# Kernel optimization log

Measured on AMD Instinct MI355X. Metric: run time of the kernel, lower is better.

Reference implementation:

```python
import jax, jax.numpy as jnp
import numpy as np

IN_F = 4096
OUT_F = 11008
N_CLUSTERS = 16
TOPK = int(IN_F * 0.25)  # 1024


def setup_inputs() -> dict:
    key = jax.random.key(0)
    k1, k2, k3, k4 = jax.random.split(key, 4)
    x = jax.random.normal(k1, (1, 1, IN_F), jnp.float32)
    weight_full = jax.random.normal(k2, (OUT_F, IN_F), jnp.float32) * 0.02
    bias_full = jax.random.normal(k3, (OUT_F,), jnp.float32) * 0.02
    # cluster centers live in softmax-activation space (compared via cdist to a softmax)
    cluster_centers = jax.nn.softmax(
        jax.random.normal(k4, (N_CLUSTERS, IN_F), jnp.float32), axis=-1)
    return {"x": x, "weight_full": weight_full, "bias_full": bias_full,
            "cluster_centers": cluster_centers}


def reference(x, weight_full, bias_full, cluster_centers):
    # hot path: bsz * seq == 1
    x_flat = x.reshape(-1, x.shape[-1])                 # [1, in]
    x_avg = jnp.abs(jnp.mean(x_flat, axis=0))           # [in]
    activation = jax.nn.softmax(x_avg, axis=0)          # [in]
    # nearest cluster center (squared L2 has same argmin as L2)
    d2 = jnp.sum((cluster_centers - activation[None, :]) ** 2, axis=-1)  # [n_clusters]
    ci = jnp.argmin(d2)
    center = cluster_centers[ci]                        # [in]
    # per-cluster precomputed top-k column indices: argsort(center, descending)[:topk]
    _, topk_idx = jax.lax.top_k(center, TOPK)           # [topk]
    x_sel = jnp.take(x_flat, topk_idx, axis=1)          # [1, topk]
    w_sel = jnp.take(weight_full, topk_idx, axis=1)     # [out, topk]
    out = x_sel @ w_sel.T + bias_full                   # [1, out]
    return out.reshape(1, 1, -1)
```

## Files before the change

### kernel.cpp

```cpp
#include <hip/hip_runtime.h>

#define IN_F 4096
#define OUT_F 11008
#define NCLUST 16
#define TOPK 1024
#define NT 1024
#define NW 16

__global__ __launch_bounds__(NT) void select_mask_kernel(
    const float* __restrict__ x,
    const float* __restrict__ centers,
    float* __restrict__ xm)
{
    const int tid  = threadIdx.x;
    const int lane = tid & 63;
    const int wid  = tid >> 6;

    __shared__ __align__(16) float sx[IN_F];
    __shared__ __align__(16) float sact[IN_F];
    __shared__ unsigned int hist[NW * 256];
    __shared__ float swred[NW];
    __shared__ float sd2[NCLUST];
    __shared__ unsigned int wtot4[4];
    __shared__ unsigned int weq[NW];
    __shared__ float smax, ssum;
    __shared__ unsigned int sprefix, sKrem, sG;
    __shared__ int sci;

    if (tid == 0) { sprefix = 0u; sKrem = TOPK; sG = 0u; }

    float4 xv = reinterpret_cast<const float4*>(x)[tid];
    reinterpret_cast<float4*>(sx)[tid] = xv;
    {
        float m = fmaxf(fmaxf(fabsf(xv.x), fabsf(xv.y)),
                        fmaxf(fabsf(xv.z), fabsf(xv.w)));
        for (int off = 32; off > 0; off >>= 1) m = fmaxf(m, __shfl_down(m, off, 64));
        if (lane == 0) swred[wid] = m;
    }
    __syncthreads();
    if (wid == 0) {
        float m = (lane < NW) ? swred[lane] : -3.0e38f;
        for (int off = 8; off > 0; off >>= 1) m = fmaxf(m, __shfl_down(m, off, 64));
        if (lane == 0) smax = m;
    }
    __syncthreads();
    const float mx = smax;

    float e0 = expf(fabsf(xv.x) - mx);
    float e1 = expf(fabsf(xv.y) - mx);
    float e2 = expf(fabsf(xv.z) - mx);
    float e3 = expf(fabsf(xv.w) - mx);
    {
        float s = e0 + e1 + e2 + e3;
        for (int off = 32; off > 0; off >>= 1) s += __shfl_down(s, off, 64);
        if (lane == 0) swred[wid] = s;
    }
    __syncthreads();
    if (wid == 0) {
        float s = (lane < NW) ? swred[lane] : 0.0f;
        for (int off = 8; off > 0; off >>= 1) s += __shfl_down(s, off, 64);
        if (lane == 0) ssum = s;
    }
    __syncthreads();
    {
        const float inv = 1.0f / ssum;
        float4 a;
        a.x = e0 * inv; a.y = e1 * inv; a.z = e2 * inv; a.w = e3 * inv;
        reinterpret_cast<float4*>(sact)[tid] = a;
    }
    __syncthreads();

    {
        const float4* c4 = reinterpret_cast<const float4*>(centers + (size_t)wid * IN_F);
        const float4* a4 = reinterpret_cast<const float4*>(sact);
        float d = 0.0f;
        #pragma unroll
        for (int it = 0; it < IN_F / 4 / 64; ++it) {
            float4 c = c4[it * 64 + lane];
            float4 a = a4[it * 64 + lane];
            float t0 = c.x - a.x, t1 = c.y - a.y, t2 = c.z - a.z, t3 = c.w - a.w;
            d += t0 * t0 + t1 * t1 + t2 * t2 + t3 * t3;
        }
        for (int off = 32; off > 0; off >>= 1) d += __shfl_down(d, off, 64);
        if (lane == 0) sd2[wid] = d;
    }
    __syncthreads();

    if (wid == 0) {
        float v = (lane < NCLUST) ? sd2[lane] : 3.0e38f;
        int   bi = lane;
        for (int off = 8; off > 0; off >>= 1) {
            float ov = __shfl_down(v, off, 64);
            int   oi = __shfl_down(bi, off, 64);
            if (ov < v) { v = ov; bi = oi; }
        }
        if (lane == 0) sci = bi;
    }
    __syncthreads();

    unsigned int cv[4];
    {
        float4 c = reinterpret_cast<const float4*>(centers + (size_t)sci * IN_F)[tid];
        cv[0] = __float_as_uint(c.x);
        cv[1] = __float_as_uint(c.y);
        cv[2] = __float_as_uint(c.z);
        cv[3] = __float_as_uint(c.w);
    }

    for (int pass = 0; pass < 4; ++pass) {
        const int shift = 24 - 8 * pass;
        for (int k = tid; k < NW * 256; k += NT) hist[k] = 0u;
        __syncthreads();
        const unsigned int pfx  = sprefix;
        const unsigned int krem = sKrem;
        unsigned int* hp = &hist[wid * 256];
        #pragma unroll
        for (int j = 0; j < 4; ++j) {
            unsigned int u = cv[j];
            bool cand = (pass == 0) || ((u >> (shift + 8)) == pfx);
            if (cand) atomicAdd(&hp[(u >> shift) & 255u], 1u);
        }
        __syncthreads();
        unsigned int h = 0, s = 0;
        if (tid < 256) {
            #pragma unroll
            for (int w = 0; w < NW; ++w) h += hist[w * 256 + tid];
            s = h;
            for (int off = 1; off < 64; off <<= 1) {
                unsigned int v2 = __shfl_down(s, off, 64);
                if (lane + off < 64) s += v2;
            }
            if (lane == 0) wtot4[wid] = s;
        }
        __syncthreads();
        if (tid < 256) {
            unsigned int add = 0;
            #pragma unroll
            for (int w = 0; w < 4; ++w) if (w > wid) add += wtot4[w];
            unsigned int incl = s + add;
            unsigned int excl = incl - h;
            if (excl < krem && krem <= incl) {
                sprefix = (pfx << 8) | (unsigned int)tid;
                sKrem   = krem - excl;
            }
        }
        __syncthreads();
    }
    const unsigned int T = sprefix;

    unsigned int gt = 0, eq = 0;
    #pragma unroll
    for (int j = 0; j < 4; ++j) {
        gt += (cv[j] > T) ? 1u : 0u;
        eq += (cv[j] == T) ? 1u : 0u;
    }
    {
        unsigned int g = gt;
        for (int off = 32; off > 0; off >>= 1) g += __shfl_down(g, off, 64);
        if (lane == 0) atomicAdd(&sG, g);
    }
    unsigned int p = eq;
    for (int off = 1; off < 64; off <<= 1) {
        unsigned int v2 = __shfl_up(p, off, 64);
        if (lane >= off) p += v2;
    }
    if (lane == 63) weq[wid] = p;
    __syncthreads();
    unsigned int base = p - eq;
    #pragma unroll
    for (int w = 0; w < NW; ++w) if (w < wid) base += weq[w];
    const unsigned int needEq = TOPK - sG;

    {
        unsigned int r = 0;
        float4 o;
        o.x = ((cv[0] > T) || ((cv[0] == T) && (base + r < needEq))) ? xv.x : 0.0f; r += (cv[0] == T);
        o.y = ((cv[1] > T) || ((cv[1] == T) && (base + r < needEq))) ? xv.y : 0.0f; r += (cv[1] == T);
        o.z = ((cv[2] > T) || ((cv[2] == T) && (base + r < needEq))) ? xv.z : 0.0f; r += (cv[2] == T);
        o.w = ((cv[3] > T) || ((cv[3] == T) && (base + r < needEq))) ? xv.w : 0.0f;
        reinterpret_cast<float4*>(xm)[tid] = o;
    }
}

__global__ __launch_bounds__(256) void matvec_kernel(
    const float* __restrict__ W,
    const float* __restrict__ xm,
    const float* __restrict__ bias,
    float* __restrict__ out)
{
    __shared__ __align__(16) float sxm[IN_F];
    const int tid = threadIdx.x;
    for (int i = tid * 4; i < IN_F; i += 256 * 4) {
        *reinterpret_cast<float4*>(&sxm[i]) =
            *reinterpret_cast<const float4*>(&xm[i]);
    }
    __syncthreads();

    const int lane = tid & 63;
    const int wid  = tid >> 6;
    const int nwaves = gridDim.x * 4;

    for (int row = blockIdx.x * 4 + wid; row < OUT_F; row += nwaves) {
        const float4* wr = reinterpret_cast<const float4*>(W + (size_t)row * IN_F);
        float acc = 0.0f;
        #pragma unroll
        for (int j = 0; j < IN_F / 4 / 64; ++j) {
            float4 w4 = wr[j * 64 + lane];
            float4 x4 = *reinterpret_cast<const float4*>(&sxm[(j * 64 + lane) * 4]);
            acc += w4.x * x4.x + w4.y * x4.y + w4.z * x4.z + w4.w * x4.w;
        }
        for (int off = 32; off > 0; off >>= 1) acc += __shfl_down(acc, off, 64);
        if (lane == 0) out[row] = acc + bias[row];
    }
}

extern "C" void kernel_launch(void* const* d_in, const int* in_sizes, int n_in,
                              void* d_out, int out_size, void* d_ws, size_t ws_size,
                              hipStream_t stream) {
    const float* x       = (const float*)d_in[0];
    const float* weight  = (const float*)d_in[1];
    const float* bias    = (const float*)d_in[2];
    const float* centers = (const float*)d_in[3];
    float* out = (float*)d_out;
    float* xm  = (float*)d_ws;

    select_mask_kernel<<<1, NT, 0, stream>>>(x, centers, xm);
    matvec_kernel<<<1376, 256, 0, stream>>>(weight, xm, bias, out);
}
```

Before: 45.65 us.

## Prefetch centers, expand cluster distance algebraically, process two rows per wave

The selection kernel now loads each wave's cluster center into registers at the start. It computes the nearest cluster as ||c||^2 - (2/sum)·c·e, using the unnormalised exponentials, which removes the softmax normalisation pass and several barriers. The chosen center is then reused from registers through shared memory instead of being re-read from global memory, and histogram clearing is moved to cut barriers. The matvec kernel has each wave compute two rows at once with independent loads, which raises memory-level parallelism in place of the strided row loop. The new launch bound with 64 float4 registers per thread risks register spills in the selection kernel, and the algebraic expansion can change rounding near ties.

```diff
diff --git a/kernel.cpp b/kernel.cpp
--- a/kernel.cpp
+++ b/kernel.cpp
@@ -7,7 +7,7 @@
 #define NT 1024
 #define NW 16
 
-__global__ __launch_bounds__(NT) void select_mask_kernel(
+__global__ __launch_bounds__(NT, 4) void select_mask_kernel(
     const float* __restrict__ x,
     const float* __restrict__ centers,
     float* __restrict__ xm)
@@ -16,21 +16,27 @@
     const int lane = tid & 63;
     const int wid  = tid >> 6;
 
-    __shared__ __align__(16) float sx[IN_F];
     __shared__ __align__(16) float sact[IN_F];
     __shared__ unsigned int hist[NW * 256];
     __shared__ float swred[NW];
-    __shared__ float sd2[NCLUST];
+    __shared__ float sdot[NCLUST];
+    __shared__ float scsq[NCLUST];
     __shared__ unsigned int wtot4[4];
     __shared__ unsigned int weq[NW];
-    __shared__ float smax, ssum;
+    __shared__ float smax;
     __shared__ unsigned int sprefix, sKrem, sG;
     __shared__ int sci;
 
     if (tid == 0) { sprefix = 0u; sKrem = TOPK; sG = 0u; }
 
     float4 xv = reinterpret_cast<const float4*>(x)[tid];
-    reinterpret_cast<float4*>(sx)[tid] = xv;
+    float4 cpre[16];
+    {
+        const float4* c4 = reinterpret_cast<const float4*>(centers + (size_t)wid * IN_F);
+        #pragma unroll
+        for (int it = 0; it < 16; ++it) cpre[it] = c4[it * 64 + lane];
+    }
+
     {
         float m = fmaxf(fmaxf(fabsf(xv.x), fabsf(xv.y)),
                         fmaxf(fabsf(xv.z), fabsf(xv.w)));
@@ -51,44 +57,38 @@
     float e2 = expf(fabsf(xv.z) - mx);
     float e3 = expf(fabsf(xv.w) - mx);
     {
+        float4 ev; ev.x = e0; ev.y = e1; ev.z = e2; ev.w = e3;
+        reinterpret_cast<float4*>(sact)[tid] = ev;
         float s = e0 + e1 + e2 + e3;
         for (int off = 32; off > 0; off >>= 1) s += __shfl_down(s, off, 64);
         if (lane == 0) swred[wid] = s;
     }
     __syncthreads();
+
+    {
+        const float4* a4 = reinterpret_cast<const float4*>(sact);
+        float dt = 0.0f, cq = 0.0f;
+        #pragma unroll
+        for (int it = 0; it < 16; ++it) {
+            float4 c = cpre[it];
+            float4 a = a4[it * 64 + lane];
+            dt += c.x * a.x + c.y * a.y + c.z * a.z + c.w * a.w;
+            cq += c.x * c.x + c.y * c.y + c.z * c.z + c.w * c.w;
+        }
+        for (int off = 32; off > 0; off >>= 1) {
+            dt += __shfl_down(dt, off, 64);
+            cq += __shfl_down(cq, off, 64);
+        }
+        if (lane == 0) { sdot[wid] = dt; scsq[wid] = cq; }
+    }
+    __syncthreads();
+
     if (wid == 0) {
         float s = (lane < NW) ? swred[lane] : 0.0f;
         for (int off = 8; off > 0; off >>= 1) s += __shfl_down(s, off, 64);
-        if (lane == 0) ssum = s;
-    }
-    __syncthreads();
-    {
-        const float inv = 1.0f / ssum;
-        float4 a;
-        a.x = e0 * inv; a.y = e1 * inv; a.z = e2 * inv; a.w = e3 * inv;
-        reinterpret_cast<float4*>(sact)[tid] = a;
-    }
-    __syncthreads();
-
-    {
-        const float4* c4 = reinterpret_cast<const float4*>(centers + (size_t)wid * IN_F);
-        const float4* a4 = reinterpret_cast<const float4*>(sact);
-        float d = 0.0f;
-        #pragma unroll
-        for (int it = 0; it < IN_F / 4 / 64; ++it) {
-            float4 c = c4[it * 64 + lane];
-            float4 a = a4[it * 64 + lane];
-            float t0 = c.x - a.x, t1 = c.y - a.y, t2 = c.z - a.z, t3 = c.w - a.w;
-            d += t0 * t0 + t1 * t1 + t2 * t2 + t3 * t3;
-        }
-        for (int off = 32; off > 0; off >>= 1) d += __shfl_down(d, off, 64);
-        if (lane == 0) sd2[wid] = d;
-    }
-    __syncthreads();
-
-    if (wid == 0) {
-        float v = (lane < NCLUST) ? sd2[lane] : 3.0e38f;
-        int   bi = lane;
+        s = __shfl(s, 0, 64);
+        float v = (lane < NCLUST) ? (scsq[lane] - (2.0f / s) * sdot[lane]) : 3.0e38f;
+        int bi = lane;
         for (int off = 8; off > 0; off >>= 1) {
             float ov = __shfl_down(v, off, 64);
             int   oi = __shfl_down(bi, off, 64);
@@ -98,9 +98,17 @@
     }
     __syncthreads();
 
+    if (wid == sci) {
+        float4* a4 = reinterpret_cast<float4*>(sact);
+        #pragma unroll
+        for (int it = 0; it < 16; ++it) a4[it * 64 + lane] = cpre[it];
+    }
+    for (int k = tid; k < NW * 256; k += NT) hist[k] = 0u;
+    __syncthreads();
+
     unsigned int cv[4];
     {
-        float4 c = reinterpret_cast<const float4*>(centers + (size_t)sci * IN_F)[tid];
+        float4 c = reinterpret_cast<const float4*>(sact)[tid];
         cv[0] = __float_as_uint(c.x);
         cv[1] = __float_as_uint(c.y);
         cv[2] = __float_as_uint(c.z);
@@ -109,8 +117,6 @@
 
     for (int pass = 0; pass < 4; ++pass) {
         const int shift = 24 - 8 * pass;
-        for (int k = tid; k < NW * 256; k += NT) hist[k] = 0u;
-        __syncthreads();
         const unsigned int pfx  = sprefix;
         const unsigned int krem = sKrem;
         unsigned int* hp = &hist[wid * 256];
@@ -145,6 +151,10 @@
             }
         }
         __syncthreads();
+        if (pass < 3) {
+            for (int k = tid; k < NW * 256; k += NT) hist[k] = 0u;
+            __syncthreads();
+        }
     }
     const unsigned int T = sprefix;
 
@@ -190,27 +200,39 @@
 {
     __shared__ __align__(16) float sxm[IN_F];
     const int tid = threadIdx.x;
-    for (int i = tid * 4; i < IN_F; i += 256 * 4) {
-        *reinterpret_cast<float4*>(&sxm[i]) =
-            *reinterpret_cast<const float4*>(&xm[i]);
+    {
+        const float4* src = reinterpret_cast<const float4*>(xm);
+        float4* dst = reinterpret_cast<float4*>(sxm);
+        #pragma unroll
+        for (int i = 0; i < IN_F / 4 / 256; ++i)
+            dst[i * 256 + tid] = src[i * 256 + tid];
     }
     __syncthreads();
 
     const int lane = tid & 63;
     const int wid  = tid >> 6;
-    const int nwaves = gridDim.x * 4;
-
-    for (int row = blockIdx.x * 4 + wid; row < OUT_F; row += nwaves) {
-        const float4* wr = reinterpret_cast<const float4*>(W + (size_t)row * IN_F);
-        float acc = 0.0f;
-        #pragma unroll
-        for (int j = 0; j < IN_F / 4 / 64; ++j) {
-            float4 w4 = wr[j * 64 + lane];
-            float4 x4 = *reinterpret_cast<const float4*>(&sxm[(j * 64 + lane) * 4]);
-            acc += w4.x * x4.x + w4.y * x4.y + w4.z * x4.z + w4.w * x4.w;
-        }
-        for (int off = 32; off > 0; off >>= 1) acc += __shfl_down(acc, off, 64);
-        if (lane == 0) out[row] = acc + bias[row];
+    const int r0 = blockIdx.x * 8 + wid * 2;
+
+    const float4* w0 = reinterpret_cast<const float4*>(W + (size_t)r0 * IN_F);
+    const float4* w1 = reinterpret_cast<const float4*>(W + (size_t)(r0 + 1) * IN_F);
+    const float4* x4 = reinterpret_cast<const float4*>(sxm);
+
+    float acc0 = 0.0f, acc1 = 0.0f;
+    #pragma unroll
+    for (int j = 0; j < IN_F / 4 / 64; ++j) {
+        float4 a = w0[j * 64 + lane];
+        float4 b = w1[j * 64 + lane];
+        float4 v = x4[j * 64 + lane];
+        acc0 += a.x * v.x + a.y * v.y + a.z * v.z + a.w * v.w;
+        acc1 += b.x * v.x + b.y * v.y + b.z * v.z + b.w * v.w;
+    }
+    for (int off = 32; off > 0; off >>= 1) {
+        acc0 += __shfl_down(acc0, off, 64);
+        acc1 += __shfl_down(acc1, off, 64);
+    }
+    if (lane == 0) {
+        out[r0]     = acc0 + bias[r0];
+        out[r0 + 1] = acc1 + bias[r0 + 1];
     }
 }
 
```

Measured after the change: 45.40 us. Within noise of the previous version (-0.5%).

## Fuse mask selection into matvec with redundant per-block selection and LDS-staged weight prefetch

Applied to the files above, without the earlier changes.

Merges the single-block selection kernel and the matvec into one 256-block kernel. Every block recomputes the softmax, nearest-center search and radix top-k itself. The cluster distance is rewritten as ||c||^2 - 2/S·(c·e), which skips the normalisation pass. Weight rows are streamed into LDS with global_load_lds double buffering and manual vmcnt waits, and the first granules are issued before the selection work so the loads overlap it. This removes a kernel launch and the serial single-block stage, at the cost of redundant selection work in every block and fragile hand-written waitcnt pipelining.

```diff
diff --git a/kernel.cpp b/kernel.cpp
--- a/kernel.cpp
+++ b/kernel.cpp
@@ -4,91 +4,134 @@
 #define OUT_F 11008
 #define NCLUST 16
 #define TOPK 1024
-#define NT 1024
-#define NW 16
-
-__global__ __launch_bounds__(NT) void select_mask_kernel(
+#define NBLK 256
+#define ROWS_PB 43
+#define GRAN_F 1024
+
+__device__ __forceinline__ float dot4(float4 a, float4 b) {
+    return a.x * b.x + a.y * b.y + a.z * b.z + a.w * b.w;
+}
+__device__ __forceinline__ float wredsum(float v) {
+    for (int o = 32; o > 0; o >>= 1) v += __shfl_down(v, o, 64);
+    return v;
+}
+__device__ __forceinline__ float wredmax(float v) {
+    for (int o = 32; o > 0; o >>= 1) v = fmaxf(v, __shfl_down(v, o, 64));
+    return v;
+}
+__device__ __forceinline__ void barrier_lds() {
+    asm volatile("s_waitcnt lgkmcnt(0)" ::: "memory");
+    __builtin_amdgcn_s_barrier();
+}
+__device__ __forceinline__ void stage_granule(const float* __restrict__ W,
+                                              int row, int q, float* lbuf,
+                                              int lane) {
+    const float* src = W + (size_t)row * IN_F + q * GRAN_F + lane * 4;
+    #pragma unroll
+    for (int j = 0; j < 4; ++j) {
+        __builtin_amdgcn_global_load_lds(
+            (const __attribute__((address_space(1))) void*)(src + j * 256),
+            (__attribute__((address_space(3))) void*)(lbuf + j * 256),
+            16, 0, 0);
+    }
+}
+
+__global__ __launch_bounds__(256, 1) void fused_kernel(
     const float* __restrict__ x,
+    const float* __restrict__ W,
+    const float* __restrict__ bias,
     const float* __restrict__ centers,
-    float* __restrict__ xm)
+    float* __restrict__ out)
 {
     const int tid  = threadIdx.x;
     const int lane = tid & 63;
     const int wid  = tid >> 6;
-
-    __shared__ __align__(16) float sx[IN_F];
-    __shared__ __align__(16) float sact[IN_F];
-    __shared__ unsigned int hist[NW * 256];
-    __shared__ float swred[NW];
-    __shared__ float sd2[NCLUST];
-    __shared__ unsigned int wtot4[4];
-    __shared__ unsigned int weq[NW];
-    __shared__ float smax, ssum;
+    const int bid  = blockIdx.x;
+
+    __shared__ __align__(16) float sxm[IN_F];
+    __shared__ __align__(16) float wstage[8][GRAN_F];
+    __shared__ unsigned int hist[4][256];
+    __shared__ float sredA[4], sredB[4];
+    __shared__ float sdot[NCLUST], scsq[NCLUST];
+    __shared__ unsigned int wtot4[4], weq[4];
     __shared__ unsigned int sprefix, sKrem, sG;
     __shared__ int sci;
 
-    if (tid == 0) { sprefix = 0u; sKrem = TOPK; sG = 0u; }
-
-    float4 xv = reinterpret_cast<const float4*>(x)[tid];
-    reinterpret_cast<float4*>(sx)[tid] = xv;
-    {
-        float m = fmaxf(fmaxf(fabsf(xv.x), fabsf(xv.y)),
-                        fmaxf(fabsf(xv.z), fabsf(xv.w)));
-        for (int off = 32; off > 0; off >>= 1) m = fmaxf(m, __shfl_down(m, off, 64));
-        if (lane == 0) swred[wid] = m;
-    }
-    __syncthreads();
+    const int nr    = (wid < 3) ? 11 : 10;
+    const int rbase = bid * ROWS_PB + wid;
+    float* buf0 = &wstage[wid * 2][0];
+    float* buf1 = &wstage[wid * 2 + 1][0];
+
+    stage_granule(W, rbase, 0, buf0, lane);
+    stage_granule(W, rbase, 1, buf1, lane);
+    asm volatile("" ::: "memory");
+
+    float4 x0 = ((const float4*)x)[tid * 4 + 0];
+    float4 x1 = ((const float4*)x)[tid * 4 + 1];
+    float4 x2 = ((const float4*)x)[tid * 4 + 2];
+    float4 x3 = ((const float4*)x)[tid * 4 + 3];
+
+    {
+        float m = fmaxf(fmaxf(fabsf(x0.x), fabsf(x0.y)), fmaxf(fabsf(x0.z), fabsf(x0.w)));
+        m = fmaxf(m, fmaxf(fmaxf(fabsf(x1.x), fabsf(x1.y)), fmaxf(fabsf(x1.z), fabsf(x1.w))));
+        m = fmaxf(m, fmaxf(fmaxf(fabsf(x2.x), fabsf(x2.y)), fmaxf(fabsf(x2.z), fabsf(x2.w))));
+        m = fmaxf(m, fmaxf(fmaxf(fabsf(x3.x), fabsf(x3.y)), fmaxf(fabsf(x3.z), fabsf(x3.w))));
+        m = wredmax(m);
+        if (lane == 0) sredA[wid] = m;
+    }
+    barrier_lds();
+    const float mx = fmaxf(fmaxf(sredA[0], sredA[1]), fmaxf(sredA[2], sredA[3]));
+
+    float e[16];
+    e[0]=expf(fabsf(x0.x)-mx); e[1]=expf(fabsf(x0.y)-mx); e[2]=expf(fabsf(x0.z)-mx); e[3]=expf(fabsf(x0.w)-mx);
+    e[4]=expf(fabsf(x1.x)-mx); e[5]=expf(fabsf(x1.y)-mx); e[6]=expf(fabsf(x1.z)-mx); e[7]=expf(fabsf(x1.w)-mx);
+    e[8]=expf(fabsf(x2.x)-mx); e[9]=expf(fabsf(x2.y)-mx); e[10]=expf(fabsf(x2.z)-mx); e[11]=expf(fabsf(x2.w)-mx);
+    e[12]=expf(fabsf(x3.x)-mx); e[13]=expf(fabsf(x3.y)-mx); e[14]=expf(fabsf(x3.z)-mx); e[15]=expf(fabsf(x3.w)-mx);
+    {
+        float4* sxm4 = (float4*)sxm;
+        sxm4[tid*4+0] = make_float4(e[0],e[1],e[2],e[3]);
+        sxm4[tid*4+1] = make_float4(e[4],e[5],e[6],e[7]);
+        sxm4[tid*4+2] = make_float4(e[8],e[9],e[10],e[11]);
+        sxm4[tid*4+3] = make_float4(e[12],e[13],e[14],e[15]);
+        float s = 0.0f;
+        #pragma unroll
+        for (int k = 0; k < 16; ++k) s += e[k];
+        s = wredsum(s);
+        if (lane == 0) sredB[wid] = s;
+    }
+    barrier_lds();
+    const float S = sredB[0] + sredB[1] + sredB[2] + sredB[3];
+
+    {
+        const float4* e4  = (const float4*)sxm;
+        const float*  cb  = centers + (size_t)(4 * wid) * IN_F;
+        const float4* c0p = (const float4*)(cb);
+        const float4* c1p = (const float4*)(cb + IN_F);
+        const float4* c2p = (const float4*)(cb + 2 * IN_F);
+        const float4* c3p = (const float4*)(cb + 3 * IN_F);
+        float d0=0,d1=0,d2=0,d3=0,q0=0,q1=0,q2=0,q3=0;
+        #pragma unroll
+        for (int j = 0; j < 16; ++j) {
+            int idx = j * 64 + lane;
+            float4 ev = e4[idx];
+            float4 a = c0p[idx], b = c1p[idx], c = c2p[idx], d = c3p[idx];
+            d0 += dot4(a, ev); q0 += dot4(a, a);
+            d1 += dot4(b, ev); q1 += dot4(b, b);
+            d2 += dot4(c, ev); q2 += dot4(c, c);
+            d3 += dot4(d, ev); q3 += dot4(d, d);
+        }
+        d0 = wredsum(d0); d1 = wredsum(d1); d2 = wredsum(d2); d3 = wredsum(d3);
+        q0 = wredsum(q0); q1 = wredsum(q1); q2 = wredsum(q2); q3 = wredsum(q3);
+        if (lane == 0) {
+            sdot[4*wid+0]=d0; sdot[4*wid+1]=d1; sdot[4*wid+2]=d2; sdot[4*wid+3]=d3;
+            scsq[4*wid+0]=q0; scsq[4*wid+1]=q1; scsq[4*wid+2]=q2; scsq[4*wid+3]=q3;
+        }
+    }
+    barrier_lds();
+
     if (wid == 0) {
-        float m = (lane < NW) ? swred[lane] : -3.0e38f;
-        for (int off = 8; off > 0; off >>= 1) m = fmaxf(m, __shfl_down(m, off, 64));
-        if (lane == 0) smax = m;
-    }
-    __syncthreads();
-    const float mx = smax;
-
-    float e0 = expf(fabsf(xv.x) - mx);
-    float e1 = expf(fabsf(xv.y) - mx);
-    float e2 = expf(fabsf(xv.z) - mx);
-    float e3 = expf(fabsf(xv.w) - mx);
-    {
-        float s = e0 + e1 + e2 + e3;
-        for (int off = 32; off > 0; off >>= 1) s += __shfl_down(s, off, 64);
-        if (lane == 0) swred[wid] = s;
-    }
-    __syncthreads();
-    if (wid == 0) {
-        float s = (lane < NW) ? swred[lane] : 0.0f;
-        for (int off = 8; off > 0; off >>= 1) s += __shfl_down(s, off, 64);
-        if (lane == 0) ssum = s;
-    }
-    __syncthreads();
-    {
-        const float inv = 1.0f / ssum;
-        float4 a;
-        a.x = e0 * inv; a.y = e1 * inv; a.z = e2 * inv; a.w = e3 * inv;
-        reinterpret_cast<float4*>(sact)[tid] = a;
-    }
-    __syncthreads();
-
-    {
-        const float4* c4 = reinterpret_cast<const float4*>(centers + (size_t)wid * IN_F);
-        const float4* a4 = reinterpret_cast<const float4*>(sact);
-        float d = 0.0f;
-        #pragma unroll
-        for (int it = 0; it < IN_F / 4 / 64; ++it) {
-            float4 c = c4[it * 64 + lane];
-            float4 a = a4[it * 64 + lane];
-            float t0 = c.x - a.x, t1 = c.y - a.y, t2 = c.z - a.z, t3 = c.w - a.w;
-            d += t0 * t0 + t1 * t1 + t2 * t2 + t3 * t3;
-        }
-        for (int off = 32; off > 0; off >>= 1) d += __shfl_down(d, off, 64);
-        if (lane == 0) sd2[wid] = d;
-    }
-    __syncthreads();
-
-    if (wid == 0) {
-        float v = (lane < NCLUST) ? sd2[lane] : 3.0e38f;
-        int   bi = lane;
+        float v = (lane < NCLUST) ? (scsq[lane] - (2.0f / S) * sdot[lane]) : 3.0e38f;
+        int bi = lane;
         for (int off = 8; off > 0; off >>= 1) {
             float ov = __shfl_down(v, off, 64);
             int   oi = __shfl_down(bi, off, 64);
@@ -96,35 +139,41 @@
         }
         if (lane == 0) sci = bi;
     }
-    __syncthreads();
-
-    unsigned int cv[4];
-    {
-        float4 c = reinterpret_cast<const float4*>(centers + (size_t)sci * IN_F)[tid];
-        cv[0] = __float_as_uint(c.x);
-        cv[1] = __float_as_uint(c.y);
-        cv[2] = __float_as_uint(c.z);
-        cv[3] = __float_as_uint(c.w);
-    }
+    barrier_lds();
+    const int ci = sci;
+
+    const float4* cc4 = (const float4*)(centers + (size_t)ci * IN_F);
+    float4 c0 = cc4[tid*4+0], c1 = cc4[tid*4+1], c2 = cc4[tid*4+2], c3 = cc4[tid*4+3];
+    {
+        unsigned int* hflat = &hist[0][0];
+        hflat[tid] = 0u; hflat[tid+256] = 0u; hflat[tid+512] = 0u; hflat[tid+768] = 0u;
+        if (tid == 0) { sprefix = 0u; sKrem = TOPK; sG = 0u; }
+    }
+    barrier_lds();
+
+    unsigned int cv[16];
+    cv[0]=__float_as_uint(c0.x); cv[1]=__float_as_uint(c0.y); cv[2]=__float_as_uint(c0.z); cv[3]=__float_as_uint(c0.w);
+    cv[4]=__float_as_uint(c1.x); cv[5]=__float_as_uint(c1.y); cv[6]=__float_as_uint(c1.z); cv[7]=__float_as_uint(c1.w);
+    cv[8]=__float_as_uint(c2.x); cv[9]=__float_as_uint(c2.y); cv[10]=__float_as_uint(c2.z); cv[11]=__float_as_uint(c2.w);
+    cv[12]=__float_as_uint(c3.x); cv[13]=__float_as_uint(c3.y); cv[14]=__float_as_uint(c3.z); cv[15]=__float_as_uint(c3.w);
 
     for (int pass = 0; pass < 4; ++pass) {
         const int shift = 24 - 8 * pass;
-        for (int k = tid; k < NW * 256; k += NT) hist[k] = 0u;
-        __syncthreads();
         const unsigned int pfx  = sprefix;
         const unsigned int krem = sKrem;
-        unsigned int* hp = &hist[wid * 256];
-        #pragma unroll
-        for (int j = 0; j < 4; ++j) {
-            unsigned int u = cv[j];
+        unsigned int* hp = hist[wid];
+        #pragma unroll
+        for (int k = 0; k < 16; ++k) {
+            unsigned int u = cv[k];
             bool cand = (pass == 0) || ((u >> (shift + 8)) == pfx);
             if (cand) atomicAdd(&hp[(u >> shift) & 255u], 1u);
         }
-        __syncthreads();
-        unsigned int h = 0, s = 0;
-        if (tid < 256) {
-            #pragma unroll
-            for (int w = 0; w < NW; ++w) h += hist[w * 256 + tid];
+        barrier_lds();
+        unsigned int h, s;
+        {
+            const unsigned int b = tid;
+            h = hist[0][b] + hist[1][b] + hist[2][b] + hist[3][b];
+            hist[0][b] = 0u; hist[1][b] = 0u; hist[2][b] = 0u; hist[3][b] = 0u;
             s = h;
             for (int off = 1; off < 64; off <<= 1) {
                 unsigned int v2 = __shfl_down(s, off, 64);
@@ -132,11 +181,11 @@
             }
             if (lane == 0) wtot4[wid] = s;
         }
-        __syncthreads();
-        if (tid < 256) {
+        barrier_lds();
+        {
             unsigned int add = 0;
             #pragma unroll
-            for (int w = 0; w < 4; ++w) if (w > wid) add += wtot4[w];
+            for (int w2 = 0; w2 < 4; ++w2) if (w2 > wid) add += wtot4[w2];
             unsigned int incl = s + add;
             unsigned int excl = incl - h;
             if (excl < krem && krem <= incl) {
@@ -144,19 +193,19 @@
                 sKrem   = krem - excl;
             }
         }
-        __syncthreads();
+        barrier_lds();
     }
     const unsigned int T = sprefix;
 
     unsigned int gt = 0, eq = 0;
     #pragma unroll
-    for (int j = 0; j < 4; ++j) {
-        gt += (cv[j] > T) ? 1u : 0u;
-        eq += (cv[j] == T) ? 1u : 0u;
+    for (int k = 0; k < 16; ++k) {
+        gt += (cv[k] > T) ? 1u : 0u;
+        eq += (cv[k] == T) ? 1u : 0u;
     }
     {
         unsigned int g = gt;
-        for (int off = 32; off > 0; off >>= 1) g += __shfl_down(g, off, 64);
+        for (int o = 32; o > 0; o >>= 1) g += __shfl_down(g, o, 64);
         if (lane == 0) atomicAdd(&sG, g);
     }
     unsigned int p = eq;
@@ -165,52 +214,63 @@
         if (lane >= off) p += v2;
     }
     if (lane == 63) weq[wid] = p;
-    __syncthreads();
+    barrier_lds();
     unsigned int base = p - eq;
     #pragma unroll
-    for (int w = 0; w < NW; ++w) if (w < wid) base += weq[w];
+    for (int w2 = 0; w2 < 4; ++w2) if (w2 < wid) base += weq[w2];
     const unsigned int needEq = TOPK - sG;
 
     {
+        float xs[16] = {x0.x,x0.y,x0.z,x0.w, x1.x,x1.y,x1.z,x1.w,
+                        x2.x,x2.y,x2.z,x2.w, x3.x,x3.y,x3.z,x3.w};
+        float os[16];
         unsigned int r = 0;
-        float4 o;
-        o.x = ((cv[0] > T) || ((cv[0] == T) && (base + r < needEq))) ? xv.x : 0.0f; r += (cv[0] == T);
-        o.y = ((cv[1] > T) || ((cv[1] == T) && (base + r < needEq))) ? xv.y : 0.0f; r += (cv[1] == T);
-        o.z = ((cv[2] > T) || ((cv[2] == T) && (base + r < needEq))) ? xv.z : 0.0f; r += (cv[2] == T);
-        o.w = ((cv[3] > T) || ((cv[3] == T) && (base + r < needEq))) ? xv.w : 0.0f;
-        reinterpret_cast<float4*>(xm)[tid] = o;
-    }
-}
-
-__global__ __launch_bounds__(256) void matvec_kernel(
-    const float* __restrict__ W,
-    const float* __restrict__ xm,
-    const float* __restrict__ bias,
-    float* __restrict__ out)
-{
-    __shared__ __align__(16) float sxm[IN_F];
-    const int tid = threadIdx.x;
-    for (int i = tid * 4; i < IN_F; i += 256 * 4) {
-        *reinterpret_cast<float4*>(&sxm[i]) =
-            *reinterpret_cast<const float4*>(&xm[i]);
-    }
-    __syncthreads();
-
-    const int lane = tid & 63;
-    const int wid  = tid >> 6;
-    const int nwaves = gridDim.x * 4;
-
-    for (int row = blockIdx.x * 4 + wid; row < OUT_F; row += nwaves) {
-        const float4* wr = reinterpret_cast<const float4*>(W + (size_t)row * IN_F);
+        #pragma unroll
+        for (int k = 0; k < 16; ++k) {
+            bool sel = (cv[k] > T) || ((cv[k] == T) && (base + r < needEq));
+            os[k] = sel ? xs[k] : 0.0f;
+            r += (cv[k] == T) ? 1u : 0u;
+        }
+        float4* sxm4 = (float4*)sxm;
+        sxm4[tid*4+0] = make_float4(os[0],os[1],os[2],os[3]);
+        sxm4[tid*4+1] = make_float4(os[4],os[5],os[6],os[7]);
+        sxm4[tid*4+2] = make_float4(os[8],os[9],os[10],os[11]);
+        sxm4[tid*4+3] = make_float4(os[12],os[13],os[14],os[15]);
+    }
+    barrier_lds();
+    float4 slice[16];
+    {
+        const float4* sxm4 = (const float4*)sxm;
+        #pragma unroll
+        for (int k = 0; k < 16; ++k) slice[k] = sxm4[k * 64 + lane];
+    }
+
+    for (int i = 0; i < nr; ++i) {
+        const int row = rbase + 4 * i;
         float acc = 0.0f;
-        #pragma unroll
-        for (int j = 0; j < IN_F / 4 / 64; ++j) {
-            float4 w4 = wr[j * 64 + lane];
-            float4 x4 = *reinterpret_cast<const float4*>(&sxm[(j * 64 + lane) * 4]);
-            acc += w4.x * x4.x + w4.y * x4.y + w4.z * x4.z + w4.w * x4.w;
-        }
-        for (int off = 32; off > 0; off >>= 1) acc += __shfl_down(acc, off, 64);
-        if (lane == 0) out[row] = acc + bias[row];
+        float bv = 0.0f;
+        #pragma unroll
+        for (int q = 0; q < 4; ++q) {
+            const int g = i * 4 + q;
+            if (g + 1 < nr * 4) { asm volatile("s_waitcnt vmcnt(4)" ::: "memory"); }
+            else                { asm volatile("s_waitcnt vmcnt(0)" ::: "memory"); }
+            if (q == 0) bv = bias[row];
+            const float4* wb = (const float4*)((q & 1) ? buf1 : buf0);
+            float4 a0 = wb[0 * 64 + lane];
+            float4 a1 = wb[1 * 64 + lane];
+            float4 a2 = wb[2 * 64 + lane];
+            float4 a3 = wb[3 * 64 + lane];
+            acc += dot4(a0, slice[q * 4 + 0]) + dot4(a1, slice[q * 4 + 1])
+                 + dot4(a2, slice[q * 4 + 2]) + dot4(a3, slice[q * 4 + 3]);
+            asm volatile("s_waitcnt lgkmcnt(0)" ::: "memory");
+            const int g2 = g + 2;
+            if (g2 < nr * 4) {
+                stage_granule(W, rbase + 4 * (g2 >> 2), g2 & 3,
+                              (g2 & 1) ? buf1 : buf0, lane);
+            }
+        }
+        for (int o = 32; o > 0; o >>= 1) acc += __shfl_down(acc, o, 64);
+        if (lane == 0) out[row] = acc + bv;
     }
 }
 
@@ -222,8 +282,6 @@
     const float* bias    = (const float*)d_in[2];
     const float* centers = (const float*)d_in[3];
     float* out = (float*)d_out;
-    float* xm  = (float*)d_ws;
-
-    select_mask_kernel<<<1, NT, 0, stream>>>(x, centers, xm);
-    matvec_kernel<<<1376, 256, 0, stream>>>(weight, xm, bias, out);
-}
+
+    fused_kernel<<<NBLK, 256, 0, stream>>>(x, weight, bias, centers, out);
+}
```

New measurement: 43.70 us. -4.3%, faster.
